# Performance work log

Measured on AMD Instinct MI355X. Metric: run time of the kernel, lower is better.

Reference implementation:

```python
import jax, jax.numpy as jnp
import numpy as np

B, SQ, SKV, D = 4, 2048, 2048, 768
H, HD = 12, 16  # num_heads, reduced head_dim (64 / reduce_factor 4)
DR = H * HD     # 192 reduced width


def setup_inputs() -> dict:
    key = jax.random.key(0)
    ks = jax.random.split(key, 6)
    s = 0.02
    return {
        "hidden_states": jax.random.normal(ks[0], (B, SQ, D), jnp.float32),
        "encoder_hidden_states": jax.random.normal(ks[1], (B, SKV, D), jnp.float32),
        "Wq": jax.random.normal(ks[2], (D, DR), jnp.float32) * s,
        "bq": jnp.zeros((DR,), jnp.float32),
        "Wkv": jax.random.normal(ks[3], (D, 2 * DR), jnp.float32) * s,
        "bkv": jnp.zeros((2 * DR,), jnp.float32),
        "Wp": jax.random.normal(ks[4], (DR, D), jnp.float32) * s,
        "bp": jnp.zeros((D,), jnp.float32),
    }


def _split_heads(x):
    # [B, S, DR] -> [B, H, S, HD]
    b, s, _ = x.shape
    return x.reshape(b, s, H, HD).transpose(0, 2, 1, 3)


def reference(hidden_states, encoder_hidden_states, Wq, bq, Wkv, bkv, Wp, bp):
    # Conv1D projections (x @ W + b)
    q = hidden_states @ Wq + bq                       # [B, SQ, 192]
    kv = encoder_hidden_states @ Wkv + bkv            # [B, SKV, 384]
    k, v = kv[..., :DR], kv[..., DR:]
    q = _split_heads(q)                               # [B, H, SQ, HD]
    k = _split_heads(k)                               # [B, H, SKV, HD]
    v = _split_heads(v)                               # [B, H, SKV, HD]
    scale = jnp.asarray(HD, q.dtype) ** 0.5
    scores = jnp.einsum('bhqd,bhkd->bhqk', q, k) / scale
    attn = jax.nn.softmax(scores, axis=-1)            # dropout is identity in eval
    out = jnp.einsum('bhqk,bhkd->bhqd', attn, v)      # [B, H, SQ, HD]
    out = out.transpose(0, 2, 1, 3).reshape(hidden_states.shape[0], -1, DR)
    out = out @ Wp + bp                               # [B, SQ, 768]
    return out
```

## Files before the change

kernel.cpp:

```cpp
#include <hip/hip_runtime.h>
#include <hip/hip_bf16.h>
#include <math.h>

#define NB 4
#define NSQ 2048
#define NSKV 2048
#define ND 768
#define NH 12
#define NHD 16
#define NDR 192
#define M_TOT (NB * NSQ)

typedef __attribute__((ext_vector_type(8)))  short          bf16x8;
typedef __attribute__((ext_vector_type(16))) float          f32x16;
typedef __attribute__((ext_vector_type(8)))  unsigned short u16x8;

__device__ __forceinline__ unsigned short bfbits(float x) {
  __hip_bfloat16 h = __float2bfloat16(x);
  unsigned short u; __builtin_memcpy(&u, &h, 2); return u;
}
__device__ __forceinline__ float bf2f(unsigned short u) {
  unsigned int v = ((unsigned int)u) << 16; float f; __builtin_memcpy(&f, &v, 4); return f;
}
__device__ __forceinline__ unsigned int pk2t(float a, float b) {
  unsigned int ua, ub;
  __builtin_memcpy(&ua, &a, 4); __builtin_memcpy(&ub, &b, 4);
#if __has_builtin(__builtin_amdgcn_perm)
  return __builtin_amdgcn_perm(ub, ua, 0x07060302);
#else
  return (ua >> 16) | (ub & 0xffff0000u);
#endif
}
__device__ __forceinline__ float exp2_raw(float x) {
#if __has_builtin(__builtin_amdgcn_exp2f)
  return __builtin_amdgcn_exp2f(x);
#else
  float r; asm("v_exp_f32 %0, %1" : "=v"(r) : "v"(x)); return r;
#endif
}
__device__ __forceinline__ void g2l16(const void* g, void* l) {
  __builtin_amdgcn_global_load_lds(
      (const __attribute__((address_space(1))) void*)g,
      (__attribute__((address_space(3))) void*)l, 16, 0, 0);
}

#define QSCALE 0.36067376022224085f
#define LDSBUF 16384

__global__ __launch_bounds__(256) void prep(
    const float* __restrict__ Wq, const float* __restrict__ Wkv,
    const float* __restrict__ Wp,
    unsigned short* __restrict__ WSq, unsigned short* __restrict__ WSkv,
    unsigned short* __restrict__ WSp) {
  int bid = blockIdx.x;
  const float* W; unsigned short* out; int Nn, KBLK, bx, by;
  if (bid < 72)        { W = Wq;  out = WSq;  Nn = 192; KBLK = 24; bx = bid % 24;        by = bid / 24; }
  else if (bid < 216)  { int b = bid - 72;  W = Wkv; out = WSkv; Nn = 384; KBLK = 24; bx = b % 24; by = b / 24; }
  else                 { int b = bid - 216; W = Wp;  out = WSp;  Nn = 768; KBLK = 6;  bx = b % 6;  by = b / 6;  }

  __shared__ float tile[32][65];
  int k0 = bx * 32, n0 = by * 64;
  int t = threadIdx.x;
  int kr = t >> 3, c0 = (t & 7) * 8;
  const float* src = W + (size_t)(k0 + kr) * Nn + n0 + c0;
  float4 f0 = *reinterpret_cast<const float4*>(src);
  float4 f1 = *reinterpret_cast<const float4*>(src + 4);
  tile[kr][c0+0] = f0.x; tile[kr][c0+1] = f0.y; tile[kr][c0+2] = f0.z; tile[kr][c0+3] = f0.w;
  tile[kr][c0+4] = f1.x; tile[kr][c0+5] = f1.y; tile[kr][c0+6] = f1.z; tile[kr][c0+7] = f1.w;
  __syncthreads();
  int n = t >> 2, cq0 = (t & 3) * 2;
  int ng = n0 + n, sw = ng & 7;
  unsigned short* dst = out + ((size_t)ng * KBLK + bx) * 64;
  #pragma unroll
  for (int q = 0; q < 2; ++q) {
    int cc = cq0 + q;
    u16x8 v;
    #pragma unroll
    for (int i = 0; i < 8; ++i) {
      float x = tile[(cc & 3) * 8 + i][n];
      unsigned short h = bfbits(x);
      v[i] = (cc < 4) ? h : bfbits(x - bf2f(h));
    }
    *reinterpret_cast<u16x8*>(dst + (cc ^ sw) * 8) = v;
  }
}

__device__ __forceinline__ void core_compute(
    const unsigned short* const (&ard)[4], const unsigned short* const (&wrd)[12],
    int off, f32x16 (&acc)[3]) {
  #pragma unroll
  for (int kk = 0; kk < 2; ++kk) {
    bf16x8 ah = *reinterpret_cast<const bf16x8*>(ard[kk*2+0] + off);
    bf16x8 al = *reinterpret_cast<const bf16x8*>(ard[kk*2+1] + off);
    #pragma unroll
    for (int nr = 0; nr < 3; ++nr) {
      bf16x8 wh = *reinterpret_cast<const bf16x8*>(wrd[(nr*2+kk)*2+0] + off);
      bf16x8 wl = *reinterpret_cast<const bf16x8*>(wrd[(nr*2+kk)*2+1] + off);
      acc[nr] = __builtin_amdgcn_mfma_f32_32x32x16_bf16(ah, wh, acc[nr], 0, 0, 0);
      acc[nr] = __builtin_amdgcn_mfma_f32_32x32x16_bf16(ah, wl, acc[nr], 0, 0, 0);
      acc[nr] = __builtin_amdgcn_mfma_f32_32x32x16_bf16(al, wh, acc[nr], 0, 0, 0);
    }
  }
}

__device__ __forceinline__ void gemm_core(
    const unsigned short* __restrict__ As,
    const unsigned short* __restrict__ Ws,
    const float* __restrict__ bias,
    int KBLK, unsigned short* lds, f32x16 (&acc)[3]) {
  const int tid = threadIdx.x;
  const int wv = tid >> 6, lane = tid & 63;
  const int l31 = lane & 31, hi8 = lane >> 5;
  const int wm = wv >> 1, wn = wv & 1;

  unsigned short* Ab = lds;
  unsigned short* Wb = lds + 64 * 64;

  const int r8 = lane >> 3, c8 = lane & 7;
  const size_t rowu = (size_t)KBLK * 64;

  const unsigned short* srcA0 = As + (size_t)((0*4 + wv)*8 + r8) * rowu + c8*8;
  const unsigned short* srcA1 = As + (size_t)((1*4 + wv)*8 + r8) * rowu + c8*8;
  const unsigned short* srcW[6];
  #pragma unroll
  for (int j = 0; j < 6; ++j)
    srcW[j] = Ws + (size_t)((j*4 + wv)*8 + r8) * rowu + c8*8;

  unsigned short* dA0 = Ab + ((0*4 + wv)*64 + lane) * 8;
  unsigned short* dA1 = Ab + ((1*4 + wv)*64 + lane) * 8;
  unsigned short* dW[6];
  #pragma unroll
  for (int j = 0; j < 6; ++j)
    dW[j] = Wb + ((j*4 + wv)*64 + lane) * 8;

  const int ra = wm*32 + l31;
  const unsigned short* ard[4];
  #pragma unroll
  for (int kk = 0; kk < 2; ++kk) {
    ard[kk*2+0] = Ab + ra*64 + (((kk*2 + hi8)     ^ (ra & 7)) * 8);
    ard[kk*2+1] = Ab + ra*64 + (((4 + kk*2 + hi8) ^ (ra & 7)) * 8);
  }
  const unsigned short* wrd[12];
  #pragma unroll
  for (int nr = 0; nr < 3; ++nr) {
    int rw = wn*96 + nr*32 + l31;
    #pragma unroll
    for (int kk = 0; kk < 2; ++kk) {
      wrd[(nr*2+kk)*2+0] = Wb + rw*64 + (((kk*2 + hi8)     ^ (rw & 7)) * 8);
      wrd[(nr*2+kk)*2+1] = Wb + rw*64 + (((4 + kk*2 + hi8) ^ (rw & 7)) * 8);
    }
  }

  #pragma unroll
  for (int nr = 0; nr < 3; ++nr) {
    float bv = bias[wn*96 + nr*32 + l31];
    #pragma unroll
    for (int r = 0; r < 16; ++r) acc[nr][r] = bv;
  }

  g2l16(srcA0, dA0); srcA0 += 64;
  g2l16(srcA1, dA1); srcA1 += 64;
  #pragma unroll
  for (int j = 0; j < 6; ++j) { g2l16(srcW[j], dW[j]); srcW[j] += 64; }
  __syncthreads();

  for (int kb = 0; kb < KBLK; kb += 2) {
    if (kb + 1 < KBLK) {
      g2l16(srcA0, dA0 + LDSBUF); srcA0 += 64;
      g2l16(srcA1, dA1 + LDSBUF); srcA1 += 64;
      #pragma unroll
      for (int j = 0; j < 6; ++j) { g2l16(srcW[j], dW[j] + LDSBUF); srcW[j] += 64; }
    }
    core_compute(ard, wrd, 0, acc);
    __syncthreads();
    if (kb + 2 < KBLK) {
      g2l16(srcA0, dA0); srcA0 += 64;
      g2l16(srcA1, dA1); srcA1 += 64;
      #pragma unroll
      for (int j = 0; j < 6; ++j) { g2l16(srcW[j], dW[j]); srcW[j] += 64; }
    }
    core_compute(ard, wrd, LDSBUF, acc);
    __syncthreads();
  }
}

__device__ __forceinline__ void gemm_core_fa(
    const float* __restrict__ Afp,
    const unsigned short* __restrict__ Ws,
    const float* __restrict__ bias,
    unsigned short* lds, f32x16 (&acc)[3]) {
  const int KBLK = ND / 32;
  const int tid = threadIdx.x;
  const int wv = tid >> 6, lane = tid & 63;
  const int l31 = lane & 31, hi8 = lane >> 5;
  const int wm = wv >> 1, wn = wv & 1;

  unsigned short* Ab = lds;
  unsigned short* Wb = lds + 64 * 64;

  const int ar = tid >> 2;
  const int cq = tid & 3;
  const float* srcA = Afp + (size_t)ar * ND + cq * 8;
  unsigned short* dAh = Ab + ar*64 + (((cq    ) ^ (ar & 7)) * 8);
  unsigned short* dAl = Ab + ar*64 + (((cq + 4) ^ (ar & 7)) * 8);

  const int r8 = lane >> 3, c8 = lane & 7;
  const size_t rowu = (size_t)KBLK * 64;
  const unsigned short* srcW[6];
  unsigned short* dW[6];
  #pragma unroll
  for (int j = 0; j < 6; ++j) {
    srcW[j] = Ws + (size_t)((j*4 + wv)*8 + r8) * rowu + c8*8;
    dW[j]   = Wb + ((j*4 + wv)*64 + lane) * 8;
  }

  const int ra = wm*32 + l31;
  const unsigned short* ard[4];
  #pragma unroll
  for (int kk = 0; kk < 2; ++kk) {
    ard[kk*2+0] = Ab + ra*64 + (((kk*2 + hi8)     ^ (ra & 7)) * 8);
    ard[kk*2+1] = Ab + ra*64 + (((4 + kk*2 + hi8) ^ (ra & 7)) * 8);
  }
  const unsigned short* wrd[12];
  #pragma unroll
  for (int nr = 0; nr < 3; ++nr) {
    int rw = wn*96 + nr*32 + l31;
    #pragma unroll
    for (int kk = 0; kk < 2; ++kk) {
      wrd[(nr*2+kk)*2+0] = Wb + rw*64 + (((kk*2 + hi8)     ^ (rw & 7)) * 8);
      wrd[(nr*2+kk)*2+1] = Wb + rw*64 + (((4 + kk*2 + hi8) ^ (rw & 7)) * 8);
    }
  }

  #pragma unroll
  for (int nr = 0; nr < 3; ++nr) {
    float bv = bias[wn*96 + nr*32 + l31];
    #pragma unroll
    for (int r = 0; r < 16; ++r) acc[nr][r] = bv;
  }

  {
    float4 f0 = *reinterpret_cast<const float4*>(srcA);
    float4 f1 = *reinterpret_cast<const float4*>(srcA + 4);
    srcA += 32;
    #pragma unroll
    for (int j = 0; j < 6; ++j) { g2l16(srcW[j], dW[j]); srcW[j] += 64; }
    float x[8] = {f0.x, f0.y, f0.z, f0.w, f1.x, f1.y, f1.z, f1.w};
    u16x8 hv, lv;
    #pragma unroll
    for (int i = 0; i < 8; ++i) {
      unsigned short h = bfbits(x[i]);
      hv[i] = h; lv[i] = bfbits(x[i] - bf2f(h));
    }
    *reinterpret_cast<u16x8*>(dAh) = hv;
    *reinterpret_cast<u16x8*>(dAl) = lv;
  }
  __syncthreads();

  for (int kb = 0; kb < KBLK; kb += 2) {
    float4 f0, f1;
    {
      f0 = *reinterpret_cast<const float4*>(srcA);
      f1 = *reinterpret_cast<const float4*>(srcA + 4);
      srcA += 32;
      #pragma unroll
      for (int j = 0; j < 6; ++j) { g2l16(srcW[j], dW[j] + LDSBUF); srcW[j] += 64; }
    }
    core_compute(ard, wrd, 0, acc);
    {
      float x[8] = {f0.x, f0.y, f0.z, f0.w, f1.x, f1.y, f1.z, f1.w};
      u16x8 hv, lv;
      #pragma unroll
      for (int i = 0; i < 8; ++i) {
        unsigned short h = bfbits(x[i]);
        hv[i] = h; lv[i] = bfbits(x[i] - bf2f(h));
      }
      *reinterpret_cast<u16x8*>(dAh + LDSBUF) = hv;
      *reinterpret_cast<u16x8*>(dAl + LDSBUF) = lv;
    }
    __syncthreads();
    bool has2 = (kb + 2 < KBLK);
    if (has2) {
      f0 = *reinterpret_cast<const float4*>(srcA);
      f1 = *reinterpret_cast<const float4*>(srcA + 4);
      srcA += 32;
      #pragma unroll
      for (int j = 0; j < 6; ++j) { g2l16(srcW[j], dW[j]); srcW[j] += 64; }
    }
    core_compute(ard, wrd, LDSBUF, acc);
    if (has2) {
      float x[8] = {f0.x, f0.y, f0.z, f0.w, f1.x, f1.y, f1.z, f1.w};
      u16x8 hv, lv;
      #pragma unroll
      for (int i = 0; i < 8; ++i) {
        unsigned short h = bfbits(x[i]);
        hv[i] = h; lv[i] = bfbits(x[i] - bf2f(h));
      }
      *reinterpret_cast<u16x8*>(dAh) = hv;
      *reinterpret_cast<u16x8*>(dAl) = lv;
    }
    __syncthreads();
  }
}

__global__ __launch_bounds__(256) void gemm_qkv(
    const float* __restrict__ A1, const float* __restrict__ A2,
    const unsigned short* __restrict__ WSq, const unsigned short* __restrict__ WSkv,
    const float* __restrict__ bq, const float* __restrict__ bkv,
    unsigned short* __restrict__ Qbf, unsigned short* __restrict__ Kbf,
    unsigned short* __restrict__ VTbf) {
  __shared__ unsigned short lds[2 * LDSBUF];
  const int bid = blockIdx.x;
  const float* Afp; const unsigned short* Ws; const float* bias;
  int m0, mode;
  if (bid < 128) {
    Afp = A1; Ws = WSq; bias = bq; m0 = bid * 64; mode = 0;
  } else {
    int b2 = bid - 128;
    int n0 = (b2 & 1) * 192;
    Afp = A2; Ws = WSkv + (size_t)n0 * (ND/32) * 64; bias = bkv + n0;
    m0 = (b2 >> 1) * 64; mode = 1 + (b2 & 1);
  }
  Afp += (size_t)m0 * ND;

  f32x16 acc[3];
  gemm_core_fa(Afp, Ws, bias, lds, acc);

  const int tid = threadIdx.x;
  const int wv = tid >> 6, lane = tid & 63;
  const int l31 = lane & 31, hi8 = lane >> 5;
  const int wm = wv >> 1, wn = wv & 1;

  if (mode == 2) {
    __syncthreads();
    unsigned short (*tile)[65] = reinterpret_cast<unsigned short(*)[65]>(lds);
    #pragma unroll
    for (int nr = 0; nr < 3; ++nr) {
      int nl = wn*96 + nr*32 + l31;
      #pragma unroll
      for (int r = 0; r < 16; ++r) {
        int col = wm*32 + (r & 3) + 8*(r >> 2) + 4*hi8;
        tile[nl][col] = bfbits(acc[nr][r]);
      }
    }
    __syncthreads();
    int b = m0 >> 11, key0 = m0 & 2047;
    #pragma unroll
    for (int i = 0; i < 6; ++i) {
      int flat = i * 256 + tid;
      int row = flat >> 3;
      int ck = flat & 7;
      int h = row >> 4, d = row & 15;
      u16x8 v;
      #pragma unroll
      for (int j = 0; j < 8; ++j) v[j] = tile[row][ck*8 + j];
      *reinterpret_cast<u16x8*>(
          &VTbf[(((size_t)(b*NH + h)*256 + (key0 >> 3) + ck)*16 + d)*8]) = v;
    }
    return;
  }

  unsigned short* outp = (mode == 0) ? Qbf : Kbf;
  const float scale = (mode == 0) ? QSCALE : 1.0f;
  #pragma unroll
  for (int nr = 0; nr < 3; ++nr) {
    int nl = wn*96 + nr*32 + l31;
    int h = nl >> 4, d = nl & 15;
    #pragma unroll
    for (int r = 0; r < 16; ++r) {
      int mg = m0 + wm*32 + (r & 3) + 8*(r >> 2) + 4*hi8;
      int b = mg >> 11, q = mg & 2047;
      outp[(((size_t)b*NH + h)*NSQ + q)*16 + d] = bfbits(acc[nr][r] * scale);
    }
  }
}

__device__ __forceinline__ void attn_tile32(
    bf16x8 qf, bf16x8 kf, bf16x8 vf0, bf16x8 vf1,
    int hi8, const f32x16& zeroc, f32x16& acc) {
  f32x16 s = __builtin_amdgcn_mfma_f32_32x32x16_bf16(kf, qf, zeroc, 0, 0, 0);

  float p[16];
  #pragma unroll
  for (int r = 0; r < 16; ++r) p[r] = exp2_raw(s[r]);

  unsigned int w[8];
  #pragma unroll
  for (int t8 = 0; t8 < 8; ++t8) w[t8] = pk2t(p[2*t8], p[2*t8+1]);

  unsigned int t0 = hi8 ? w[0] : w[2], t1 = hi8 ? w[1] : w[3];
  unsigned int t2 = hi8 ? w[4] : w[6], t3 = hi8 ? w[5] : w[7];
  unsigned int r0 = (unsigned int)__shfl_xor((int)t0, 32);
  unsigned int r1 = (unsigned int)__shfl_xor((int)t1, 32);
  unsigned int r2 = (unsigned int)__shfl_xor((int)t2, 32);
  unsigned int r3 = (unsigned int)__shfl_xor((int)t3, 32);

  union { bf16x8 v; unsigned int u[4]; } pa0, pa1;
  pa0.u[0] = hi8 ? r0 : w[0];  pa0.u[1] = hi8 ? r1 : w[1];
  pa0.u[2] = hi8 ? w[2] : r0;  pa0.u[3] = hi8 ? w[3] : r1;
  pa1.u[0] = hi8 ? r2 : w[4];  pa1.u[1] = hi8 ? r3 : w[5];
  pa1.u[2] = hi8 ? w[6] : r2;  pa1.u[3] = hi8 ? w[7] : r3;

  __builtin_amdgcn_s_setprio(1);
  acc = __builtin_amdgcn_mfma_f32_32x32x16_bf16(vf0, pa0.v, acc, 0, 0, 0);
  acc = __builtin_amdgcn_mfma_f32_32x32x16_bf16(vf1, pa1.v, acc, 0, 0, 0);
  __builtin_amdgcn_s_setprio(0);
}

__global__ __launch_bounds__(256, 4) void attn_bf16(
    const unsigned short* __restrict__ Qbf, const unsigned short* __restrict__ Kbf,
    const unsigned short* __restrict__ VT, unsigned short* __restrict__ AOS) {
  __shared__ float comb[4][64][9];
  const int tid = threadIdx.x;
  const int wave = tid >> 6, lane = tid & 63;
  const int l31 = lane & 31, hi8 = lane >> 5;
  const int bid = blockIdx.x;
  const int qt = bid & 63;
  const int bh = bid >> 6;
  const int q = qt * 32 + l31;

  bf16x8 qf = *reinterpret_cast<const bf16x8*>(&Qbf[((size_t)bh*NSQ + q)*16 + hi8*8]);
  const unsigned short* kbase = Kbf + (size_t)bh * NSKV * 16;

  const short fillv = (l31 == 16) ? (short)0x3F80 : (short)0;
  bf16x8 vfill;
  #pragma unroll
  for (int j = 0; j < 8; ++j) vfill[j] = fillv;

  f32x16 acc;
  #pragma unroll
  for (int r = 0; r < 16; ++r) acc[r] = 0.f;
  const f32x16 zeroc = acc;

  const int kstart = wave * (NSKV / 4);
  const unsigned short* kp = &kbase[(size_t)(kstart + l31)*16 + hi8*8];
  const unsigned short* vwave = VT + ((((size_t)bh*256 + (kstart >> 3) + hi8)*16 + l31) * 8);

  bf16x8 k0, v00, v10;
  bf16x8 k1, v01, v11;

  k0  = *reinterpret_cast<const bf16x8*>(kp);
  v00 = vfill; v10 = vfill;
  if (l31 < 16) {
    v00 = *reinterpret_cast<const bf16x8*>(vwave);
    v10 = *reinterpret_cast<const bf16x8*>(vwave + 256);
  }

  for (int kt = 0; kt < 512; kt += 64) {
    {
      k1 = *reinterpret_cast<const bf16x8*>(kp + (size_t)(kt + 32) * 16);
      v01 = vfill; v11 = vfill;
      if (l31 < 16) {
        const unsigned short* vq = vwave + (size_t)(kt + 32) * 16;
        v01 = *reinterpret_cast<const bf16x8*>(vq);
        v11 = *reinterpret_cast<const bf16x8*>(vq + 256);
      }
    }
    attn_tile32(qf, k0, v00, v10, hi8, zeroc, acc);
    if (kt + 64 < 512) {
      k0 = *reinterpret_cast<const bf16x8*>(kp + (size_t)(kt + 64) * 16);
      v00 = vfill; v10 = vfill;
      if (l31 < 16) {
        const unsigned short* vq = vwave + (size_t)(kt + 64) * 16;
        v00 = *reinterpret_cast<const bf16x8*>(vq);
        v10 = *reinterpret_cast<const bf16x8*>(vq + 256);
      }
    }
    attn_tile32(qf, k1, v01, v11, hi8, zeroc, acc);
  }

  {
    float* cb = &comb[wave][lane][0];
    #pragma unroll
    for (int r = 0; r < 9; ++r) cb[r] = acc[r];
  }
  __syncthreads();

  if (wave == 0) {
    float A[9];
    #pragma unroll
    for (int r = 0; r < 9; ++r)
      A[r] = ((comb[0][lane][r] + comb[1][lane][r]) +
              (comb[2][lane][r] + comb[3][lane][r]));
    float L = A[8] + __shfl_xor(A[8], 32);
    float inv = 1.f / L;

    unsigned short oh[8], ol[8];
    #pragma unroll
    for (int r = 0; r < 8; ++r) {
      float o = A[r] * inv;
      oh[r] = bfbits(o);
      ol[r] = bfbits(o - bf2f(oh[r]));
    }
    int b = bh / NH, h = bh % NH;
    int mrow = b * NSQ + q;
    unsigned short* rowp = AOS + (size_t)mrow * (6 * 64);
    int sw = mrow & 7;
    int kblk = h >> 1;
    int cA = (h & 1) * 2;
    unsigned short* p0;
    p0 = rowp + ((kblk*8 + ((cA + 0) ^ sw)) * 8) + 4*hi8;
    reinterpret_cast<unsigned int*>(p0)[0] = (unsigned)oh[0] | ((unsigned)oh[1] << 16);
    reinterpret_cast<unsigned int*>(p0)[1] = (unsigned)oh[2] | ((unsigned)oh[3] << 16);
    p0 = rowp + ((kblk*8 + ((cA + 1) ^ sw)) * 8) + 4*hi8;
    reinterpret_cast<unsigned int*>(p0)[0] = (unsigned)oh[4] | ((unsigned)oh[5] << 16);
    reinterpret_cast<unsigned int*>(p0)[1] = (unsigned)oh[6] | ((unsigned)oh[7] << 16);
    p0 = rowp + ((kblk*8 + ((cA + 4) ^ sw)) * 8) + 4*hi8;
    reinterpret_cast<unsigned int*>(p0)[0] = (unsigned)ol[0] | ((unsigned)ol[1] << 16);
    reinterpret_cast<unsigned int*>(p0)[1] = (unsigned)ol[2] | ((unsigned)ol[3] << 16);
    p0 = rowp + ((kblk*8 + ((cA + 5) ^ sw)) * 8) + 4*hi8;
    reinterpret_cast<unsigned int*>(p0)[0] = (unsigned)ol[4] | ((unsigned)ol[5] << 16);
    reinterpret_cast<unsigned int*>(p0)[1] = (unsigned)ol[6] | ((unsigned)ol[7] << 16);
  }
}

__global__ __launch_bounds__(256) void gemm_out_k(
    const unsigned short* __restrict__ AOS, const unsigned short* __restrict__ WSp,
    const float* __restrict__ bp, float* __restrict__ out) {
  __shared__ unsigned short lds[2 * LDSBUF];
  const int bid = blockIdx.x;
  const int KBLK = NDR / 32;
  int m0 = (bid >> 2) * 64;
  int n0 = (bid & 3) * 192;
  const unsigned short* As = AOS + (size_t)m0 * KBLK * 64;
  const unsigned short* Ws = WSp + (size_t)n0 * KBLK * 64;
  f32x16 acc[3];
  gemm_core(As, Ws, bp + n0, KBLK, lds, acc);

  const int tid = threadIdx.x;
  const int wv = tid >> 6, lane = tid & 63;
  const int l31 = lane & 31, hi8 = lane >> 5;
  const int wm = wv >> 1, wn = wv & 1;
  #pragma unroll
  for (int nr = 0; nr < 3; ++nr) {
    int n = n0 + wn*96 + nr*32 + l31;
    #pragma unroll
    for (int r = 0; r < 16; ++r) {
      int mg = m0 + wm*32 + (r & 3) + 8*(r >> 2) + 4*hi8;
      out[(size_t)mg * ND + n] = acc[nr][r];
    }
  }
}

extern "C" void kernel_launch(void* const* d_in, const int* in_sizes, int n_in,
                              void* d_out, int out_size, void* d_ws, size_t ws_size,
                              hipStream_t stream) {
  const float* hs  = (const float*)d_in[0];
  const float* ehs = (const float*)d_in[1];
  const float* Wq  = (const float*)d_in[2];
  const float* bq  = (const float*)d_in[3];
  const float* Wkv = (const float*)d_in[4];
  const float* bkv = (const float*)d_in[5];
  const float* Wp  = (const float*)d_in[6];
  const float* bp  = (const float*)d_in[7];
  float* out = (float*)d_out;

  char* w = (char*)d_ws;
  unsigned short* AOS = (unsigned short*)w;
  char* w2 = w + (size_t)M_TOT * 6 * 64 * 2;
  unsigned short* WSq  = (unsigned short*)w2;
  unsigned short* WSkv = (unsigned short*)(w2 + 589824);
  unsigned short* WSp  = (unsigned short*)(w2 + 589824 + 1179648);
  char* w3 = w2 + 589824 + 1179648 + 589824;
  unsigned short* Qbf  = (unsigned short*)w3;
  unsigned short* Kbf  = Qbf + (size_t)M_TOT * NDR;
  unsigned short* VTbf = Kbf + (size_t)M_TOT * NDR;

  prep<<<dim3(72 + 144 + 72), dim3(256), 0, stream>>>(
      Wq, Wkv, Wp, WSq, WSkv, WSp);
  gemm_qkv<<<dim3(384), dim3(256), 0, stream>>>(hs, ehs, WSq, WSkv, bq, bkv, Qbf, Kbf, VTbf);
  attn_bf16<<<dim3(NB * NH * 64), dim3(256), 0, stream>>>(Qbf, Kbf, VTbf, AOS);
  gemm_out_k<<<dim3(512), dim3(256), 0, stream>>>(AOS, WSp, bp, out);
}
```

Baseline: 92.29 us.

## Split QKV GEMM into 64x96 tiles with 6-wave blocks and doubled grid

The QKV projection kernel is retiled. Each block now computes a 64x96 output tile with 384 threads (six waves, one 32x32 accumulator each) instead of a 64x192 tile with 256 threads. This doubles the grid from 384 to 768 blocks, giving the GPU more blocks to spread across its compute units. The cost is that each A row tile is now loaded and split into hi/lo bf16 twice, once per N half, and only 256 of the 384 threads take part in the A staging.

```diff
diff --git a/kernel.cpp b/kernel.cpp
--- a/kernel.cpp
+++ b/kernel.cpp
@@ -184,111 +184,78 @@
   }
 }
 
-__device__ __forceinline__ void gemm_core_fa(
-    const float* __restrict__ Afp,
-    const unsigned short* __restrict__ Ws,
-    const float* __restrict__ bias,
-    unsigned short* lds, f32x16 (&acc)[3]) {
-  const int KBLK = ND / 32;
+#define QHALF 10240
+__global__ __launch_bounds__(384) void gemm_qkv(
+    const float* __restrict__ A1, const float* __restrict__ A2,
+    const unsigned short* __restrict__ WSq, const unsigned short* __restrict__ WSkv,
+    const float* __restrict__ bq, const float* __restrict__ bkv,
+    unsigned short* __restrict__ Qbf, unsigned short* __restrict__ Kbf,
+    unsigned short* __restrict__ VTbf) {
+  __shared__ unsigned short lds[2 * QHALF];
+  const int bid = blockIdx.x;
+  const float* Afp; const unsigned short* Ws; const float* bias;
+  int m0, mode, ntile;
+  if (bid < 256) {
+    mode = 0; ntile = (bid & 1) * 96;
+    Afp = A1; Ws = WSq + (size_t)ntile * (24*64); bias = bq + ntile;
+    m0 = (bid >> 1) * 64;
+  } else {
+    int b2 = bid - 256;
+    int sub = b2 & 3;
+    m0 = (b2 >> 2) * 64;
+    Afp = A2;
+    if (sub < 2) { mode = 1; ntile = sub * 96;
+                   Ws = WSkv + (size_t)ntile * (24*64); bias = bkv + ntile; }
+    else         { mode = 2; ntile = (sub - 2) * 96;
+                   Ws = WSkv + (size_t)(192 + ntile) * (24*64); bias = bkv + 192 + ntile; }
+  }
+  Afp += (size_t)m0 * ND;
+
   const int tid = threadIdx.x;
   const int wv = tid >> 6, lane = tid & 63;
   const int l31 = lane & 31, hi8 = lane >> 5;
-  const int wm = wv >> 1, wn = wv & 1;
+  const int wm = wv & 1, wn = wv >> 1;
 
   unsigned short* Ab = lds;
-  unsigned short* Wb = lds + 64 * 64;
-
-  const int ar = tid >> 2;
-  const int cq = tid & 3;
-  const float* srcA = Afp + (size_t)ar * ND + cq * 8;
-  unsigned short* dAh = Ab + ar*64 + (((cq    ) ^ (ar & 7)) * 8);
-  unsigned short* dAl = Ab + ar*64 + (((cq + 4) ^ (ar & 7)) * 8);
-
-  const int r8 = lane >> 3, c8 = lane & 7;
-  const size_t rowu = (size_t)KBLK * 64;
-  const unsigned short* srcW[6];
-  unsigned short* dW[6];
-  #pragma unroll
-  for (int j = 0; j < 6; ++j) {
-    srcW[j] = Ws + (size_t)((j*4 + wv)*8 + r8) * rowu + c8*8;
-    dW[j]   = Wb + ((j*4 + wv)*64 + lane) * 8;
-  }
+  unsigned short* Wb = lds + 64*64;
+
+  const int ar = tid >> 2, cq = tid & 3;
+  const bool doA = (tid < 256);
+  const float* srcA = Afp + (size_t)(doA ? ar : 0) * ND + cq*8;
+  unsigned short* dAh = Ab + (doA ? ar : 0)*64 + ((cq       ^ (ar & 7)) * 8);
+  unsigned short* dAl = Ab + (doA ? ar : 0)*64 + (((cq + 4) ^ (ar & 7)) * 8);
+
+  const int wch0 = tid, wch1 = tid + 384;
+  const unsigned short* srcW0 = Ws + (size_t)(wch0 >> 3) * (24*64) + (wch0 & 7) * 8;
+  const unsigned short* srcW1 = Ws + (size_t)(wch1 >> 3) * (24*64) + (wch1 & 7) * 8;
+  unsigned short* dW0 = Wb + wch0 * 8;
+  unsigned short* dW1 = Wb + wch1 * 8;
 
   const int ra = wm*32 + l31;
+  const int rw = wn*32 + l31;
   const unsigned short* ard[4];
+  const unsigned short* wrd[4];
   #pragma unroll
   for (int kk = 0; kk < 2; ++kk) {
     ard[kk*2+0] = Ab + ra*64 + (((kk*2 + hi8)     ^ (ra & 7)) * 8);
     ard[kk*2+1] = Ab + ra*64 + (((4 + kk*2 + hi8) ^ (ra & 7)) * 8);
-  }
-  const unsigned short* wrd[12];
-  #pragma unroll
-  for (int nr = 0; nr < 3; ++nr) {
-    int rw = wn*96 + nr*32 + l31;
-    #pragma unroll
-    for (int kk = 0; kk < 2; ++kk) {
-      wrd[(nr*2+kk)*2+0] = Wb + rw*64 + (((kk*2 + hi8)     ^ (rw & 7)) * 8);
-      wrd[(nr*2+kk)*2+1] = Wb + rw*64 + (((4 + kk*2 + hi8) ^ (rw & 7)) * 8);
-    }
-  }
-
-  #pragma unroll
-  for (int nr = 0; nr < 3; ++nr) {
-    float bv = bias[wn*96 + nr*32 + l31];
-    #pragma unroll
-    for (int r = 0; r < 16; ++r) acc[nr][r] = bv;
-  }
-
+    wrd[kk*2+0] = Wb + rw*64 + (((kk*2 + hi8)     ^ (rw & 7)) * 8);
+    wrd[kk*2+1] = Wb + rw*64 + (((4 + kk*2 + hi8) ^ (rw & 7)) * 8);
+  }
+
+  f32x16 acc;
   {
-    float4 f0 = *reinterpret_cast<const float4*>(srcA);
-    float4 f1 = *reinterpret_cast<const float4*>(srcA + 4);
-    srcA += 32;
-    #pragma unroll
-    for (int j = 0; j < 6; ++j) { g2l16(srcW[j], dW[j]); srcW[j] += 64; }
-    float x[8] = {f0.x, f0.y, f0.z, f0.w, f1.x, f1.y, f1.z, f1.w};
-    u16x8 hv, lv;
-    #pragma unroll
-    for (int i = 0; i < 8; ++i) {
-      unsigned short h = bfbits(x[i]);
-      hv[i] = h; lv[i] = bfbits(x[i] - bf2f(h));
-    }
-    *reinterpret_cast<u16x8*>(dAh) = hv;
-    *reinterpret_cast<u16x8*>(dAl) = lv;
-  }
-  __syncthreads();
-
-  for (int kb = 0; kb < KBLK; kb += 2) {
-    float4 f0, f1;
-    {
-      f0 = *reinterpret_cast<const float4*>(srcA);
-      f1 = *reinterpret_cast<const float4*>(srcA + 4);
-      srcA += 32;
-      #pragma unroll
-      for (int j = 0; j < 6; ++j) { g2l16(srcW[j], dW[j] + LDSBUF); srcW[j] += 64; }
-    }
-    core_compute(ard, wrd, 0, acc);
-    {
-      float x[8] = {f0.x, f0.y, f0.z, f0.w, f1.x, f1.y, f1.z, f1.w};
-      u16x8 hv, lv;
-      #pragma unroll
-      for (int i = 0; i < 8; ++i) {
-        unsigned short h = bfbits(x[i]);
-        hv[i] = h; lv[i] = bfbits(x[i] - bf2f(h));
-      }
-      *reinterpret_cast<u16x8*>(dAh + LDSBUF) = hv;
-      *reinterpret_cast<u16x8*>(dAl + LDSBUF) = lv;
-    }
-    __syncthreads();
-    bool has2 = (kb + 2 < KBLK);
-    if (has2) {
-      f0 = *reinterpret_cast<const float4*>(srcA);
-      f1 = *reinterpret_cast<const float4*>(srcA + 4);
-      srcA += 32;
-      #pragma unroll
-      for (int j = 0; j < 6; ++j) { g2l16(srcW[j], dW[j]); srcW[j] += 64; }
-    }
-    core_compute(ard, wrd, LDSBUF, acc);
-    if (has2) {
+    float bv = bias[wn*32 + l31];
+    #pragma unroll
+    for (int r = 0; r < 16; ++r) acc[r] = bv;
+  }
+
+  {
+    g2l16(srcW0, dW0); srcW0 += 64;
+    g2l16(srcW1, dW1); srcW1 += 64;
+    if (doA) {
+      float4 f0 = *reinterpret_cast<const float4*>(srcA);
+      float4 f1 = *reinterpret_cast<const float4*>(srcA + 4);
       float x[8] = {f0.x, f0.y, f0.z, f0.w, f1.x, f1.y, f1.z, f1.w};
       u16x8 hv, lv;
       #pragma unroll
@@ -299,61 +266,91 @@
       *reinterpret_cast<u16x8*>(dAh) = hv;
       *reinterpret_cast<u16x8*>(dAl) = lv;
     }
+    srcA += 32;
+  }
+  __syncthreads();
+
+  #define QKV_COMPUTE(off)                                                     \
+    {                                                                          \
+      _Pragma("unroll")                                                        \
+      for (int kk = 0; kk < 2; ++kk) {                                         \
+        bf16x8 ah = *reinterpret_cast<const bf16x8*>(ard[kk*2+0] + (off));     \
+        bf16x8 al = *reinterpret_cast<const bf16x8*>(ard[kk*2+1] + (off));     \
+        bf16x8 wh = *reinterpret_cast<const bf16x8*>(wrd[kk*2+0] + (off));     \
+        bf16x8 wl = *reinterpret_cast<const bf16x8*>(wrd[kk*2+1] + (off));     \
+        acc = __builtin_amdgcn_mfma_f32_32x32x16_bf16(ah, wh, acc, 0, 0, 0);   \
+        acc = __builtin_amdgcn_mfma_f32_32x32x16_bf16(ah, wl, acc, 0, 0, 0);   \
+        acc = __builtin_amdgcn_mfma_f32_32x32x16_bf16(al, wh, acc, 0, 0, 0);   \
+      }                                                                        \
+    }
+
+  for (int kb = 0; kb < 24; kb += 2) {
+    float4 f0, f1;
+    g2l16(srcW0, dW0 + QHALF); srcW0 += 64;
+    g2l16(srcW1, dW1 + QHALF); srcW1 += 64;
+    if (doA) {
+      f0 = *reinterpret_cast<const float4*>(srcA);
+      f1 = *reinterpret_cast<const float4*>(srcA + 4);
+    }
+    srcA += 32;
+    QKV_COMPUTE(0)
+    if (doA) {
+      float x[8] = {f0.x, f0.y, f0.z, f0.w, f1.x, f1.y, f1.z, f1.w};
+      u16x8 hv, lv;
+      #pragma unroll
+      for (int i = 0; i < 8; ++i) {
+        unsigned short h = bfbits(x[i]);
+        hv[i] = h; lv[i] = bfbits(x[i] - bf2f(h));
+      }
+      *reinterpret_cast<u16x8*>(dAh + QHALF) = hv;
+      *reinterpret_cast<u16x8*>(dAl + QHALF) = lv;
+    }
     __syncthreads();
-  }
-}
-
-__global__ __launch_bounds__(256) void gemm_qkv(
-    const float* __restrict__ A1, const float* __restrict__ A2,
-    const unsigned short* __restrict__ WSq, const unsigned short* __restrict__ WSkv,
-    const float* __restrict__ bq, const float* __restrict__ bkv,
-    unsigned short* __restrict__ Qbf, unsigned short* __restrict__ Kbf,
-    unsigned short* __restrict__ VTbf) {
-  __shared__ unsigned short lds[2 * LDSBUF];
-  const int bid = blockIdx.x;
-  const float* Afp; const unsigned short* Ws; const float* bias;
-  int m0, mode;
-  if (bid < 128) {
-    Afp = A1; Ws = WSq; bias = bq; m0 = bid * 64; mode = 0;
-  } else {
-    int b2 = bid - 128;
-    int n0 = (b2 & 1) * 192;
-    Afp = A2; Ws = WSkv + (size_t)n0 * (ND/32) * 64; bias = bkv + n0;
-    m0 = (b2 >> 1) * 64; mode = 1 + (b2 & 1);
-  }
-  Afp += (size_t)m0 * ND;
-
-  f32x16 acc[3];
-  gemm_core_fa(Afp, Ws, bias, lds, acc);
-
-  const int tid = threadIdx.x;
-  const int wv = tid >> 6, lane = tid & 63;
-  const int l31 = lane & 31, hi8 = lane >> 5;
-  const int wm = wv >> 1, wn = wv & 1;
+    bool has2 = (kb + 2 < 24);
+    if (has2) {
+      g2l16(srcW0, dW0); srcW0 += 64;
+      g2l16(srcW1, dW1); srcW1 += 64;
+      if (doA) {
+        f0 = *reinterpret_cast<const float4*>(srcA);
+        f1 = *reinterpret_cast<const float4*>(srcA + 4);
+      }
+      srcA += 32;
+    }
+    QKV_COMPUTE(QHALF)
+    if (has2 && doA) {
+      float x[8] = {f0.x, f0.y, f0.z, f0.w, f1.x, f1.y, f1.z, f1.w};
+      u16x8 hv, lv;
+      #pragma unroll
+      for (int i = 0; i < 8; ++i) {
+        unsigned short h = bfbits(x[i]);
+        hv[i] = h; lv[i] = bfbits(x[i] - bf2f(h));
+      }
+      *reinterpret_cast<u16x8*>(dAh) = hv;
+      *reinterpret_cast<u16x8*>(dAl) = lv;
+    }
+    __syncthreads();
+  }
+  #undef QKV_COMPUTE
 
   if (mode == 2) {
-    __syncthreads();
     unsigned short (*tile)[65] = reinterpret_cast<unsigned short(*)[65]>(lds);
     #pragma unroll
-    for (int nr = 0; nr < 3; ++nr) {
-      int nl = wn*96 + nr*32 + l31;
-      #pragma unroll
-      for (int r = 0; r < 16; ++r) {
-        int col = wm*32 + (r & 3) + 8*(r >> 2) + 4*hi8;
-        tile[nl][col] = bfbits(acc[nr][r]);
-      }
+    for (int r = 0; r < 16; ++r) {
+      int key_l = wm*32 + (r & 3) + 8*(r >> 2) + 4*hi8;
+      tile[wn*32 + l31][key_l] = bfbits(acc[r]);
     }
     __syncthreads();
     int b = m0 >> 11, key0 = m0 & 2047;
     #pragma unroll
-    for (int i = 0; i < 6; ++i) {
-      int flat = i * 256 + tid;
+    for (int j = 0; j < 2; ++j) {
+      int flat = j * 384 + tid;
       int row = flat >> 3;
       int ck = flat & 7;
-      int h = row >> 4, d = row & 15;
+      int vcol = ntile + row;
+      int h = vcol >> 4, d = vcol & 15;
       u16x8 v;
       #pragma unroll
-      for (int j = 0; j < 8; ++j) v[j] = tile[row][ck*8 + j];
+      for (int jj = 0; jj < 8; ++jj) v[jj] = tile[row][ck*8 + jj];
       *reinterpret_cast<u16x8*>(
           &VTbf[(((size_t)(b*NH + h)*256 + (key0 >> 3) + ck)*16 + d)*8]) = v;
     }
@@ -362,15 +359,14 @@
 
   unsigned short* outp = (mode == 0) ? Qbf : Kbf;
   const float scale = (mode == 0) ? QSCALE : 1.0f;
-  #pragma unroll
-  for (int nr = 0; nr < 3; ++nr) {
-    int nl = wn*96 + nr*32 + l31;
-    int h = nl >> 4, d = nl & 15;
+  {
+    int col = ntile + wn*32 + l31;
+    int h = col >> 4, d = col & 15;
     #pragma unroll
     for (int r = 0; r < 16; ++r) {
       int mg = m0 + wm*32 + (r & 3) + 8*(r >> 2) + 4*hi8;
       int b = mg >> 11, q = mg & 2047;
-      outp[(((size_t)b*NH + h)*NSQ + q)*16 + d] = bfbits(acc[nr][r] * scale);
+      outp[(((size_t)b*NH + h)*NSQ + q)*16 + d] = bfbits(acc[r] * scale);
     }
   }
 }
@@ -568,7 +564,7 @@
 
   prep<<<dim3(72 + 144 + 72), dim3(256), 0, stream>>>(
       Wq, Wkv, Wp, WSq, WSkv, WSp);
-  gemm_qkv<<<dim3(384), dim3(256), 0, stream>>>(hs, ehs, WSq, WSkv, bq, bkv, Qbf, Kbf, VTbf);
+  gemm_qkv<<<dim3(768), dim3(384), 0, stream>>>(hs, ehs, WSq, WSkv, bq, bkv, Qbf, Kbf, VTbf);
   attn_bf16<<<dim3(NB * NH * 64), dim3(256), 0, stream>>>(Qbf, Kbf, VTbf, AOS);
   gemm_out_k<<<dim3(512), dim3(256), 0, stream>>>(AOS, WSp, bp, out);
 }
```

After: 89.08 us (median of 2 runs). -3.5%, faster.
